# Optimization experiments

Measured on AMD Instinct MI355X. Metric: run time of the kernel, lower is better.

The kernel has to match this reference:

```python
import jax, jax.numpy as jnp
import numpy as np

B, T_ENC, T_DEC = 64, 100, 50
L = 512      # lstm_size
E = 512      # input_encoding_size
H = 512      # att_hidden_size
R = 8        # num_review_steps
V_TOK = 30001  # token_cnt + 1 embedding rows
V_OUT = 30000  # word_cnt


def _lstm_maxout(s, c):
    # ARNet/neuraltalk2 LSTMCore: 5*L preactivations, maxout input transform
    i = jax.nn.sigmoid(s[:, :L])
    f = jax.nn.sigmoid(s[:, L:2 * L])
    o = jax.nn.sigmoid(s[:, 2 * L:3 * L])
    t = jnp.maximum(s[:, 3 * L:4 * L], s[:, 4 * L:])
    c2 = f * c + i * t
    return o * jnp.tanh(c2), c2


def _attend(feats, h, Wa2a, ba2a, Wh2a, bh2a, Watt, batt):
    # feats: [B, A, F], h: [B, L] -> context [B, F]
    p = jnp.tanh(feats @ Wa2a + ba2a + (h @ Wh2a + bh2a)[:, None, :])  # [B,A,H]
    e = jnp.squeeze(p @ Watt, -1) + batt                               # [B,A]
    a = jax.nn.softmax(e, axis=-1)
    return jnp.einsum('ba,baf->bf', a, feats)


def setup_inputs() -> dict:
    key = jax.random.key(0)
    ks = iter(jax.random.split(key, 48))
    g = lambda shape: jax.random.normal(next(ks), shape, jnp.float32) * 0.05
    z = lambda shape: jnp.zeros(shape, jnp.float32)
    return {
        'code_matrix': jax.random.randint(next(ks), (B, T_ENC), 0, V_TOK),
        'comment_matrix': jax.random.randint(next(ks), (B, T_DEC), 0, V_TOK),
        'current_comment_mask_cuda': jnp.ones((B, T_DEC), jnp.float32),
        'embed': jax.random.uniform(next(ks), (V_TOK, E), jnp.float32, -0.1, 0.1),
        'enc_Wi': g((E, 5 * L)), 'enc_bi': z((5 * L,)),
        'enc_Wh': g((L, 5 * L)), 'enc_bh': z((5 * L,)),
        'rev_Wh': g((R, L, 5 * L)), 'rev_bh': z((R, 5 * L)),
        'rev_Wa': g((R, L, 5 * L)), 'rev_ba': z((R, 5 * L)),
        'rev_Wa2a': g((R, L, H)), 'rev_ba2a': z((R, H)),
        'rev_Wh2a': g((R, L, H)), 'rev_bh2a': z((R, H)),
        'rev_Watt': g((R, H, 1)), 'rev_batt': z((R,)),
        'dec_Wi': g((E, 5 * L)), 'dec_bi': z((5 * L,)),
        'dec_Wh': g((L, 5 * L)), 'dec_bh': z((5 * L,)),
        'dec_Wa': g((L, 5 * L)), 'dec_ba': z((5 * L,)),
        'dec_Wa2a': g((L, H)), 'dec_ba2a': z((H,)),
        'dec_Wh2a': g((L, H)), 'dec_bh2a': z((H,)),
        'dec_Watt': g((H, 1)), 'dec_batt': z(()),
        'logit_W': jax.random.uniform(next(ks), (L, V_OUT), jnp.float32, -0.1, 0.1),
        'logit_b': z((V_OUT,)),
    }


def reference(code_matrix, comment_matrix, current_comment_mask_cuda, embed,
              enc_Wi, enc_bi, enc_Wh, enc_bh,
              rev_Wh, rev_bh, rev_Wa, rev_ba, rev_Wa2a, rev_ba2a,
              rev_Wh2a, rev_bh2a, rev_Watt, rev_batt,
              dec_Wi, dec_bi, dec_Wh, dec_bh, dec_Wa, dec_ba,
              dec_Wa2a, dec_ba2a, dec_Wh2a, dec_bh2a, dec_Watt, dec_batt,
              logit_W, logit_b):
    del current_comment_mask_cuda  # only used by scheduled sampling (ss_prob=0)
    Bsz = code_matrix.shape[0]
    h0 = jnp.zeros((Bsz, L), embed.dtype)
    c0 = jnp.zeros((Bsz, L), embed.dtype)

    # ---- encode ----
    enc_x = embed[code_matrix]  # [B, T_enc, E]

    def enc_step(carry, xt):
        h, c = carry
        s = xt @ enc_Wi + enc_bi + h @ enc_Wh + enc_bh
        h2, c2 = _lstm_maxout(s, c)
        return (h2, c2), h2

    (h_enc, c_enc), enc_hs = jax.lax.scan(enc_step, (h0, c0), jnp.swapaxes(enc_x, 0, 1))
    enc_hs = jnp.swapaxes(enc_hs, 0, 1)  # [B, T_enc, L]

    # ---- review (distinct params per step; scan over stacked params) ----
    def rev_step(carry, p):
        h, c = carry
        Wh, bh, Wa, ba, Wa2a, ba2a, Wh2a, bh2a, Watt, batt = p
        att_v = _attend(enc_hs, h, Wa2a, ba2a, Wh2a, bh2a, Watt, batt)
        s = h @ Wh + bh + att_v @ Wa + ba
        h2, c2 = _lstm_maxout(s, c)
        return (h2, c2), h2

    rev_params = (rev_Wh, rev_bh, rev_Wa, rev_ba, rev_Wa2a, rev_ba2a,
                  rev_Wh2a, rev_bh2a, rev_Watt, rev_batt)
    _, thought = jax.lax.scan(rev_step, (h_enc, c_enc), rev_params)
    thought = jnp.swapaxes(thought, 0, 1)  # [B, R, L]

    # ---- decode (teacher forcing; decode_state starts from encode_state) ----
    dec_x = embed[comment_matrix]  # [B, T_dec, E]

    def dec_step(carry, xt):
        h, c = carry
        att_v = _attend(thought, h, dec_Wa2a, dec_ba2a, dec_Wh2a, dec_bh2a, dec_Watt, dec_batt)
        s = xt @ dec_Wi + dec_bi + h @ dec_Wh + dec_bh + att_v @ dec_Wa + dec_ba
        h2, c2 = _lstm_maxout(s, c)
        logp = jax.nn.log_softmax(h2 @ logit_W + logit_b, axis=-1)
        return (h2, c2), logp

    _, logps = jax.lax.scan(dec_step, (h_enc, c_enc), jnp.swapaxes(dec_x, 0, 1))
    return jnp.swapaxes(logps, 0, 1)  # [B, T_dec, V_OUT]
```

## Files before the change

kernel.cpp:

```cpp
#include <hip/hip_runtime.h>
#include <math.h>
#include <stdint.h>

#define BB     64
#define TENC   100
#define TDEC   50
#define LDIM   512
#define EE     512
#define HDIM   512
#define FIVEL  2560
#define RSTEPS 8
#define VOUT   30000
#define NB2    470

typedef __attribute__((ext_vector_type(8))) short short8v;
typedef __attribute__((ext_vector_type(4))) float floatx4;
typedef unsigned short ushort_t;

static const size_t OFF_A        = 0;
static const size_t OFF_WIT_ENC  = 8192000;
static const size_t OFF_ENCX     = 8847360;
static const size_t OFF_LOGWT    = 0;
static const size_t OFF_DECH     = 7680000;
static const size_t OFF_DECPRE   = 8499200;
static const size_t OFF_ENC_HS   = 13107200;
static const size_t OFF_ENC_WHT  = 14745600;
static const size_t OFF_REVWC    = 15400960;
static const size_t OFF_PART     = 15400960;
static const size_t OFF_DECWC    = 25886720;
static const size_t OFF_WIT_DEC  = 27197440;
static const size_t OFF_REVWT    = 27852800;
static const size_t OFF_DECWT    = 28901376;
static const size_t OFF_REVWH2AT = 29032448;
static const size_t OFF_DECWH2AT = 30081024;
static const size_t OFF_DECX     = 30212096;
static const size_t OFF_THOUGHT  = 31031296;
static const size_t OFF_TPROJ    = 31162368;
static const size_t OFF_HB0      = 31293440;
static const size_t OFF_HB1      = 31309824;
static const size_t OFF_ATTV     = 31326208;
static const size_t OFF_H0       = 31342592;
static const size_t OFF_C0       = 31358976;
static const size_t OFF_SBUF     = 31490048;
static const size_t WS_TOTAL     = 31653888;

__device__ __forceinline__ float sigmoidf_(float x) { return 1.0f / (1.0f + __expf(-x)); }
__device__ __forceinline__ float tanh_fast(float x) { return 1.0f - 2.0f / (__expf(2.0f * x) + 1.0f); }
__device__ __forceinline__ unsigned short f2bf(float x) {
    unsigned u = __float_as_uint(x);
    u += 0x7FFFu + ((u >> 16) & 1u);
    return (unsigned short)(u >> 16);
}
__device__ __forceinline__ float bf2f(unsigned short h) {
    return __uint_as_float(((unsigned)h) << 16);
}

__global__ __launch_bounds__(128)
void gather_embed(const float* __restrict__ embed, const int* __restrict__ tok,
                  int T, ushort_t* __restrict__ X)
{
    int m = blockIdx.x, t = m / BB, b = m % BB;
    const float* src = embed + (size_t)tok[b * T + t] * EE;
    float4 v = *(const float4*)(src + threadIdx.x * 4);
    ushort4 o = { f2bf(v.x), f2bf(v.y), f2bf(v.z), f2bf(v.w) };
    *(ushort4*)(X + (size_t)m * EE + threadIdx.x * 4) = o;
}

__global__ __launch_bounds__(256)
void conv_transpose(const float* __restrict__ W, ushort_t* __restrict__ WT,
                    int N, int ldWT, int kofs, long Wz, long WTz)
{
    W  += (size_t)blockIdx.z * Wz;
    WT += (size_t)blockIdx.z * WTz;
    __shared__ float tile[32][33];
    int n0 = blockIdx.x * 32, k0 = blockIdx.y * 32;
    int tx = threadIdx.x & 31, ty = threadIdx.x >> 5;
    #pragma unroll
    for (int i = 0; i < 4; ++i) {
        int k = k0 + ty + i * 8, n = n0 + tx;
        tile[ty + i * 8][tx] = (n < N) ? W[(size_t)k * N + n] : 0.f;
    }
    __syncthreads();
    #pragma unroll
    for (int i = 0; i < 4; ++i) {
        int n = n0 + ty + i * 8, k = k0 + tx;
        if (n < N) WT[(size_t)n * ldWT + kofs + k] = f2bf(tile[tx][ty + i * 8]);
    }
}

__global__ __launch_bounds__(256)
void gemm_bf16(const ushort_t* __restrict__ A, const ushort_t* __restrict__ BT,
               const float* __restrict__ bias, ushort_t* __restrict__ Cb,
               int N, int K, long ldc)
{
    __shared__ ushort_t lds[2][128][32];
    __shared__ ushort_t ctile[128 * 128];
    const int tid  = threadIdx.x;
    const int wave = tid >> 6, lane = tid & 63;
    const int m0 = blockIdx.y * 128, n0 = blockIdx.x * 128;
    const int wr = wave >> 1, wc = wave & 1;

    floatx4 acc[4][4] = {};
    const int sr  = lane >> 2;
    const int scp = lane & 3;

    for (int k0 = 0; k0 < K; k0 += 32) {
        #pragma unroll
        for (int half = 0; half < 2; ++half) {
            int rbase = wave * 32 + half * 16;
            int r = rbase + sr;
            int c = scp ^ ((r >> 1) & 3);
            const ushort_t* ga = A + (size_t)(m0 + r) * K + k0 + c * 8;
            const ushort_t* gb = BT + (size_t)(n0 + r) * K + k0 + c * 8;
            __builtin_amdgcn_global_load_lds(
                (const __attribute__((address_space(1))) void*)ga,
                (__attribute__((address_space(3))) void*)&lds[0][rbase][0], 16, 0, 0);
            __builtin_amdgcn_global_load_lds(
                (const __attribute__((address_space(1))) void*)gb,
                (__attribute__((address_space(3))) void*)&lds[1][rbase][0], 16, 0, 0);
        }
        __syncthreads();

        short8v af[4], bv[4];
        #pragma unroll
        for (int i = 0; i < 4; ++i) {
            int ra = wr * 64 + i * 16 + (lane & 15);
            int ca = (lane >> 4) ^ ((ra >> 1) & 3);
            af[i] = *(const short8v*)&lds[0][ra][ca * 8];
            int rb = wc * 64 + i * 16 + (lane & 15);
            int cb = (lane >> 4) ^ ((rb >> 1) & 3);
            bv[i] = *(const short8v*)&lds[1][rb][cb * 8];
        }
        #pragma unroll
        for (int i = 0; i < 4; ++i)
            #pragma unroll
            for (int j = 0; j < 4; ++j)
                acc[i][j] = __builtin_amdgcn_mfma_f32_16x16x32_bf16(af[i], bv[j], acc[i][j], 0, 0, 0);
        __syncthreads();
    }

    const int crow0 = wr * 64 + (lane >> 4) * 4;
    const int ccol0 = wc * 64 + (lane & 15);
    #pragma unroll
    for (int i = 0; i < 4; ++i) {
        #pragma unroll
        for (int j = 0; j < 4; ++j) {
            int col = ccol0 + j * 16;
            float bval = bias ? bias[n0 + col] : 0.f;
            #pragma unroll
            for (int rr = 0; rr < 4; ++rr)
                ctile[(crow0 + i * 16 + rr) * 128 + col] = f2bf(acc[i][j][rr] + bval);
        }
    }
    __syncthreads();
    #pragma unroll
    for (int itc = 0; itc < 8; ++itc) {
        int chunk = itc * 256 + tid;
        int row = chunk >> 4, ch = chunk & 15;
        *(short8v*)(Cb + (size_t)(m0 + row) * ldc + n0 + ch * 8) =
            *(const short8v*)&ctile[row * 128 + ch * 8];
    }
}

__global__ __launch_bounds__(256)
void gemm_logit(const ushort_t* __restrict__ A, const ushort_t* __restrict__ BT,
                const float* __restrict__ bias, float* __restrict__ C,
                float2* __restrict__ part, int N, int K)
{
    __shared__ ushort_t lds[2][128][32];
    __shared__ float ctf[128 * 128];
    const int tid  = threadIdx.x;
    const int wave = tid >> 6, lane = tid & 63;
    const int m0 = blockIdx.y * 128, n0 = blockIdx.x * 128;
    const int wr = wave >> 1, wc = wave & 1;

    floatx4 acc[4][4] = {};
    const int sr  = lane >> 2;
    const int scp = lane & 3;

    for (int k0 = 0; k0 < K; k0 += 32) {
        #pragma unroll
        for (int half = 0; half < 2; ++half) {
            int rbase = wave * 32 + half * 16;
            int r = rbase + sr;
            int c = scp ^ ((r >> 1) & 3);
            const ushort_t* ga = A + (size_t)(m0 + r) * K + k0 + c * 8;
            int nr = n0 + r; if (nr >= N) nr = 0;
            const ushort_t* gb = BT + (size_t)nr * K + k0 + c * 8;
            __builtin_amdgcn_global_load_lds(
                (const __attribute__((address_space(1))) void*)ga,
                (__attribute__((address_space(3))) void*)&lds[0][rbase][0], 16, 0, 0);
            __builtin_amdgcn_global_load_lds(
                (const __attribute__((address_space(1))) void*)gb,
                (__attribute__((address_space(3))) void*)&lds[1][rbase][0], 16, 0, 0);
        }
        __syncthreads();

        short8v af[4], bv[4];
        #pragma unroll
        for (int i = 0; i < 4; ++i) {
            int ra = wr * 64 + i * 16 + (lane & 15);
            int ca = (lane >> 4) ^ ((ra >> 1) & 3);
            af[i] = *(const short8v*)&lds[0][ra][ca * 8];
            int rb = wc * 64 + i * 16 + (lane & 15);
            int cb = (lane >> 4) ^ ((rb >> 1) & 3);
            bv[i] = *(const short8v*)&lds[1][rb][cb * 8];
        }
        #pragma unroll
        for (int i = 0; i < 4; ++i)
            #pragma unroll
            for (int j = 0; j < 4; ++j)
                acc[i][j] = __builtin_amdgcn_mfma_f32_16x16x32_bf16(af[i], bv[j], acc[i][j], 0, 0, 0);
        __syncthreads();
    }

    const int cn = lane & 15, qq = lane >> 4;
    const int lcol0 = wc * 64 + cn;
    float bv[4]; bool valid[4];
    #pragma unroll
    for (int j = 0; j < 4; ++j) {
        int col = n0 + lcol0 + j * 16;
        valid[j] = col < N;
        bv[j] = valid[j] ? bias[col] : 0.f;
    }
    const int nb2 = blockIdx.x * 2 + wc;
    #pragma unroll
    for (int i = 0; i < 4; ++i) {
        #pragma unroll
        for (int rr = 0; rr < 4; ++rr) {
            int lrow = wr * 64 + qq * 4 + i * 16 + rr;
            int m = m0 + lrow;
            float v[4];
            #pragma unroll
            for (int j = 0; j < 4; ++j)
                v[j] = valid[j] ? acc[i][j][rr] + bv[j] : -3.0e38f;
            float mx = fmaxf(fmaxf(v[0], v[1]), fmaxf(v[2], v[3]));
            #pragma unroll
            for (int msk = 1; msk < 16; msk <<= 1) mx = fmaxf(mx, __shfl_xor(mx, msk));
            float sm = 0.f;
            #pragma unroll
            for (int j = 0; j < 4; ++j) if (valid[j]) sm += __expf(v[j] - mx);
            #pragma unroll
            for (int msk = 1; msk < 16; msk <<= 1) sm += __shfl_xor(sm, msk);
            if (cn == 0) part[(size_t)m * NB2 + nb2] = make_float2(mx, sm);
            #pragma unroll
            for (int j = 0; j < 4; ++j)
                ctf[lrow * 128 + lcol0 + j * 16] = v[j];
        }
    }
    __syncthreads();
    #pragma unroll
    for (int itc = 0; itc < 16; ++itc) {
        int chunk = itc * 256 + tid;
        int row = chunk >> 5, ch = chunk & 31;
        int col = n0 + ch * 4;
        if (col < N) {
            int m = m0 + row;
            int t = m >> 6, bb = m & 63;
            float* dst = C + ((size_t)bb * TDEC + t) * VOUT + col;
            if (col + 3 < N) {
                *(floatx4*)dst = *(const floatx4*)&ctf[row * 128 + ch * 4];
            } else {
                for (int e = 0; e < 4 && col + e < N; ++e)
                    dst[e] = ctf[row * 128 + ch * 4 + e];
            }
        }
    }
}

__global__ __launch_bounds__(256)
void logsm_sub(float* __restrict__ out, const float2* __restrict__ part)
{
    const int r = blockIdx.x;
    const int b = r / TDEC, t = r % TDEC;
    const int m = t * 64 + b;
    const int tid = threadIdx.x, wave = tid >> 6, lane = tid & 63;
    float M = -3.0e38f, S = 0.f;
    for (int i = tid; i < NB2; i += 256) {
        float2 p = part[(size_t)m * NB2 + i];
        float nm = fmaxf(M, p.x);
        S = S * __expf(M - nm) + p.y * __expf(p.x - nm);
        M = nm;
    }
    #pragma unroll
    for (int off = 32; off; off >>= 1) {
        float Mo = __shfl_xor(M, off), So = __shfl_xor(S, off);
        float nm = fmaxf(M, Mo);
        S = S * __expf(M - nm) + So * __expf(Mo - nm);
        M = nm;
    }
    __shared__ float ms[4], ss[4];
    if (lane == 0) { ms[wave] = M; ss[wave] = S; }
    __syncthreads();
    float M2 = fmaxf(fmaxf(ms[0], ms[1]), fmaxf(ms[2], ms[3]));
    float S2 = ss[0] * __expf(ms[0] - M2) + ss[1] * __expf(ms[1] - M2) +
               ss[2] * __expf(ms[2] - M2) + ss[3] * __expf(ms[3] - M2);
    float lse = M2 + __logf(S2);
    floatx4* row = (floatx4*)(out + (size_t)r * VOUT);
    for (int i = tid; i < VOUT / 4; i += 256) {
        floatx4 x = __builtin_nontemporal_load(row + i);
        x[0] -= lse; x[1] -= lse; x[2] -= lse; x[3] -= lse;
        __builtin_nontemporal_store(x, row + i);
    }
}

template<int NSEG>
__global__ __launch_bounds__(256)
void step_gemm(const ushort_t* __restrict__ a0, const ushort_t* __restrict__ a1,
               const ushort_t* __restrict__ BT, int ldBT, float* __restrict__ sbuf)
{
    constexpr int K = NSEG * 512;
    constexpr int LROW = K + 8;
    __shared__ ushort_t Bl[16 * LROW];
    const int tid = threadIdx.x, wave = tid >> 6, lane = tid & 63;
    const int q = lane >> 4, cn = lane & 15;
    const int n0 = blockIdx.x * 16;

    #pragma unroll
    for (int it = 0; it < NSEG * 4; ++it) {
        int slot = it * 4 + wave;
        int row  = slot / NSEG;
        int part = slot % NSEG;
        const ushort_t* src = BT + (size_t)(n0 + row) * ldBT + part * 512 + lane * 8;
        __builtin_amdgcn_global_load_lds(
            (const __attribute__((address_space(1))) void*)src,
            (__attribute__((address_space(3))) void*)&Bl[row * LROW + part * 512], 16, 0, 0);
    }
    __syncthreads();

    floatx4 acc = {0.f, 0.f, 0.f, 0.f};
    {
        const ushort_t* Ap = a0 + (size_t)(wave * 16 + cn) * 512 + q * 8;
        #pragma unroll
        for (int kt = 0; kt < 16; ++kt) {
            short8v af = *(const short8v*)(Ap + kt * 32);
            short8v bf = *(const short8v*)&Bl[cn * LROW + kt * 32 + q * 8];
            acc = __builtin_amdgcn_mfma_f32_16x16x32_bf16(af, bf, acc, 0, 0, 0);
        }
    }
    if (NSEG == 2) {
        const ushort_t* Ap = a1 + (size_t)(wave * 16 + cn) * 512 + q * 8;
        #pragma unroll
        for (int kt = 0; kt < 16; ++kt) {
            short8v af = *(const short8v*)(Ap + kt * 32);
            short8v bf = *(const short8v*)&Bl[cn * LROW + 512 + kt * 32 + q * 8];
            acc = __builtin_amdgcn_mfma_f32_16x16x32_bf16(af, bf, acc, 0, 0, 0);
        }
    }
    #pragma unroll
    for (int rr = 0; rr < 4; ++rr)
        sbuf[(size_t)(wave * 16 + q * 4 + rr) * FIVEL + n0 + cn] = acc[rr];
}

__global__ __launch_bounds__(256)
void lstm_epi(const float* __restrict__ s, const ushort_t* __restrict__ pre,
              const float* __restrict__ b0, const float* __restrict__ b1,
              const float* __restrict__ c_in, float* __restrict__ c_out,
              ushort_t* __restrict__ h_out, ushort_t* __restrict__ h_copy)
{
    int idx = blockIdx.x * 256 + threadIdx.x;
    int row = idx >> 8;
    int c   = (idx & 255) * 2;
    float sg[5][2];
    #pragma unroll
    for (int g = 0; g < 5; ++g) {
        float2 v = *(const float2*)(s + (size_t)row * FIVEL + g * 512 + c);
        sg[g][0] = v.x + b0[g * 512 + c];
        sg[g][1] = v.y + b0[g * 512 + c + 1];
        if (b1) {
            sg[g][0] += b1[g * 512 + c];
            sg[g][1] += b1[g * 512 + c + 1];
        }
        if (pre) {
            ushort2 p = *(const ushort2*)(pre + (size_t)row * FIVEL + g * 512 + c);
            sg[g][0] += bf2f(p.x);
            sg[g][1] += bf2f(p.y);
        }
    }
    float2 ci = *(const float2*)(c_in + (size_t)row * 512 + c);
    float cc[2] = {ci.x, ci.y};
    ushort_t hh[2];
    #pragma unroll
    for (int e = 0; e < 2; ++e) {
        float ig = sigmoidf_(sg[0][e]), fg = sigmoidf_(sg[1][e]), og = sigmoidf_(sg[2][e]);
        float tt = fmaxf(sg[3][e], sg[4][e]);
        float c2 = fg * cc[e] + ig * tt;
        cc[e] = c2;
        hh[e] = f2bf(og * tanh_fast(c2));
    }
    *(float2*)(c_out + (size_t)row * 512 + c) = make_float2(cc[0], cc[1]);
    ushort2 ho = {hh[0], hh[1]};
    *(ushort2*)(h_out + (size_t)row * 512 + c) = ho;
    if (h_copy) *(ushort2*)(h_copy + (size_t)row * 512 + c) = ho;
}

__global__ __launch_bounds__(256)
void attfuse2(const ushort_t* __restrict__ hprev,
              const ushort_t* __restrict__ projBase, long projLd,
              const ushort_t* __restrict__ feats,
              const ushort_t* __restrict__ W2aT, const float* __restrict__ b2a,
              const float* __restrict__ Watt, ushort_t* __restrict__ attv, int A)
{
    __shared__ float hp[512];
    __shared__ float ealpha[128];
    const int b = blockIdx.x;
    const int tid = threadIdx.x, wave = tid >> 6, lane = tid & 63;
    const int q = lane >> 4, cn = lane & 15;

    floatx4 acc[8] = {};
    {
        const ushort_t* Ap = hprev + (size_t)b * 512 + q * 8;
        const ushort_t* Bp = W2aT + (size_t)(wave * 128 + cn) * 512 + q * 8;
        #pragma unroll 2
        for (int kt = 0; kt < 16; ++kt) {
            short8v af = *(const short8v*)(Ap + kt * 32);
            #pragma unroll
            for (int t8 = 0; t8 < 8; ++t8) {
                short8v bf = *(const short8v*)(Bp + (size_t)t8 * 16 * 512 + kt * 32);
                acc[t8] = __builtin_amdgcn_mfma_f32_16x16x32_bf16(af, bf, acc[t8], 0, 0, 0);
            }
        }
    }
    if (q == 0) {
        #pragma unroll
        for (int t8 = 0; t8 < 8; ++t8) {
            int n = wave * 128 + t8 * 16 + cn;
            hp[n] = acc[t8][0] + b2a[n];
        }
    }
    __syncthreads();

    float hpr[8], war[8];
    {
        float4 w0 = *(const float4*)(Watt + lane * 8);
        float4 w1 = *(const float4*)(Watt + lane * 8 + 4);
        war[0] = w0.x; war[1] = w0.y; war[2] = w0.z; war[3] = w0.w;
        war[4] = w1.x; war[5] = w1.y; war[6] = w1.z; war[7] = w1.w;
        #pragma unroll
        for (int j = 0; j < 8; ++j) hpr[j] = hp[lane * 8 + j];
    }

    for (int a = wave; a < A; a += 4) {
        short8v pv = *(const short8v*)(projBase + ((size_t)a * 64 + b) * projLd + lane * 8);
        float e = 0.f;
        #pragma unroll
        for (int j = 0; j < 8; ++j)
            e += tanh_fast(bf2f((ushort_t)pv[j]) + hpr[j]) * war[j];
        #pragma unroll
        for (int off = 32; off; off >>= 1) e += __shfl_xor(e, off);
        if (lane == 0) ealpha[a] = e;
    }
    __syncthreads();
    if (wave == 0) {
        float v1 = (lane < A) ? ealpha[lane] : -3.0e38f;
        float v2 = (lane + 64 < A) ? ealpha[lane + 64] : -3.0e38f;
        float mm = fmaxf(v1, v2);
        #pragma unroll
        for (int off = 32; off; off >>= 1) mm = fmaxf(mm, __shfl_xor(mm, off));
        float x1 = (lane < A) ? __expf(v1 - mm) : 0.f;
        float x2 = (lane + 64 < A) ? __expf(v2 - mm) : 0.f;
        float ss = x1 + x2;
        #pragma unroll
        for (int off = 32; off; off >>= 1) ss += __shfl_xor(ss, off);
        float inv = 1.f / ss;
        if (lane < A) ealpha[lane] = x1 * inv;
        if (lane + 64 < A) ealpha[lane + 64] = x2 * inv;
    }
    __syncthreads();

    float s0 = 0.f, s1 = 0.f;
    for (int a = 0; a < A; ++a) {
        float al = ealpha[a];
        unsigned int u = *(const unsigned int*)(feats + ((size_t)a * 64 + b) * 512 + tid * 2);
        s0 += al * bf2f((ushort_t)(u & 0xffffu));
        s1 += al * bf2f((ushort_t)(u >> 16));
    }
    ushort2 o = { f2bf(s0), f2bf(s1) };
    *(ushort2*)(attv + (size_t)b * 512 + tid * 2) = o;
}

extern "C" void kernel_launch(void* const* d_in, const int* in_sizes, int n_in,
                              void* d_out_, int out_size, void* d_ws, size_t ws_size,
                              hipStream_t stream)
{
    const int*   code     = (const int*)  d_in[0];
    const int*   comment  = (const int*)  d_in[1];
    const float* embed    = (const float*)d_in[3];
    const float* enc_Wi   = (const float*)d_in[4];
    const float* enc_bi   = (const float*)d_in[5];
    const float* enc_Wh   = (const float*)d_in[6];
    const float* enc_bh   = (const float*)d_in[7];
    const float* rev_Wh   = (const float*)d_in[8];
    const float* rev_bh   = (const float*)d_in[9];
    const float* rev_Wa   = (const float*)d_in[10];
    const float* rev_ba   = (const float*)d_in[11];
    const float* rev_Wa2a = (const float*)d_in[12];
    const float* rev_ba2a = (const float*)d_in[13];
    const float* rev_Wh2a = (const float*)d_in[14];
    const float* rev_bh2a = (const float*)d_in[15];
    const float* rev_Watt = (const float*)d_in[16];
    const float* dec_Wi   = (const float*)d_in[18];
    const float* dec_bi   = (const float*)d_in[19];
    const float* dec_Wh   = (const float*)d_in[20];
    const float* dec_bh   = (const float*)d_in[21];
    const float* dec_Wa   = (const float*)d_in[22];
    const float* dec_ba   = (const float*)d_in[23];
    const float* dec_Wa2a = (const float*)d_in[24];
    const float* dec_ba2a = (const float*)d_in[25];
    const float* dec_Wh2a = (const float*)d_in[26];
    const float* dec_bh2a = (const float*)d_in[27];
    const float* dec_Watt = (const float*)d_in[28];
    const float* logit_W  = (const float*)d_in[30];
    const float* logit_b  = (const float*)d_in[31];
    float* out = (float*)d_out_;

    float* ws = (float*)d_ws;
    if (ws_size < WS_TOTAL * sizeof(float)) return;

    ushort_t* enc_pre_b = (ushort_t*)(ws + OFF_A);
    ushort_t* rev_projA = (ushort_t*)(ws + OFF_A);
    ushort_t* logit_WT  = (ushort_t*)(ws + OFF_LOGWT);
    ushort_t* dec_h_b   = (ushort_t*)(ws + OFF_DECH);
    ushort_t* dec_pre_b = (ushort_t*)(ws + OFF_DECPRE);
    ushort_t* WiT_enc   = (ushort_t*)(ws + OFF_WIT_ENC);
    ushort_t* enc_x_b   = (ushort_t*)(ws + OFF_ENCX);
    ushort_t* enc_hs_b  = (ushort_t*)(ws + OFF_ENC_HS);
    ushort_t* encWhT    = (ushort_t*)(ws + OFF_ENC_WHT);
    ushort_t* revWcomb  = (ushort_t*)(ws + OFF_REVWC);
    float2*   part      = (float2*)(ws + OFF_PART);
    ushort_t* decWcomb  = (ushort_t*)(ws + OFF_DECWC);
    ushort_t* WiT_dec   = (ushort_t*)(ws + OFF_WIT_DEC);
    ushort_t* revWT     = (ushort_t*)(ws + OFF_REVWT);
    ushort_t* decWT     = (ushort_t*)(ws + OFF_DECWT);
    ushort_t* revWh2aT  = (ushort_t*)(ws + OFF_REVWH2AT);
    ushort_t* decWh2aT  = (ushort_t*)(ws + OFF_DECWH2AT);
    ushort_t* dec_x_b   = (ushort_t*)(ws + OFF_DECX);
    ushort_t* thought_b = (ushort_t*)(ws + OFF_THOUGHT);
    ushort_t* tproj_b   = (ushort_t*)(ws + OFF_TPROJ);
    ushort_t* hb[2] = { (ushort_t*)(ws + OFF_HB0), (ushort_t*)(ws + OFF_HB1) };
    ushort_t* attv_b    = (ushort_t*)(ws + OFF_ATTV);
    ushort_t* h0_b      = (ushort_t*)(ws + OFF_H0);
    float*    sbuf      = ws + OFF_SBUF;
    float* cbuf[4];
    for (int i = 0; i < 4; ++i) cbuf[i] = ws + OFF_C0 + (size_t)i * 32768;

    const dim3 blk(256);

    (void)hipMemsetAsync(cbuf[0], 0, (size_t)BB * LDIM * sizeof(float), stream);
    (void)hipMemsetAsync(h0_b, 0, (size_t)BB * LDIM * sizeof(ushort_t), stream);

    gather_embed<<<TENC * BB, 128, 0, stream>>>(embed, code, TENC, enc_x_b);
    gather_embed<<<TDEC * BB, 128, 0, stream>>>(embed, comment, TDEC, dec_x_b);
    conv_transpose<<<dim3(80, 16, 1), blk, 0, stream>>>(enc_Wi, WiT_enc, FIVEL, 512, 0, 0, 0);
    conv_transpose<<<dim3(80, 16, 1), blk, 0, stream>>>(enc_Wh, encWhT, FIVEL, 512, 0, 0, 0);
    conv_transpose<<<dim3(80, 16, 8), blk, 0, stream>>>(rev_Wh, revWcomb, FIVEL, 1024, 0,   1310720, 2621440);
    conv_transpose<<<dim3(80, 16, 8), blk, 0, stream>>>(rev_Wa, revWcomb, FIVEL, 1024, 512, 1310720, 2621440);
    conv_transpose<<<dim3(16, 16, 8), blk, 0, stream>>>(rev_Wa2a, revWT, 512, 512, 0,       262144, 262144);
    conv_transpose<<<dim3(16, 16, 8), blk, 0, stream>>>(rev_Wh2a, revWh2aT, 512, 512, 0,    262144, 262144);
    conv_transpose<<<dim3(80, 16, 1), blk, 0, stream>>>(dec_Wi, WiT_dec, FIVEL, 512, 0, 0, 0);
    conv_transpose<<<dim3(80, 16, 1), blk, 0, stream>>>(dec_Wh, decWcomb, FIVEL, 1024, 0, 0, 0);
    conv_transpose<<<dim3(80, 16, 1), blk, 0, stream>>>(dec_Wa, decWcomb, FIVEL, 1024, 512, 0, 0);
    conv_transpose<<<dim3(16, 16, 1), blk, 0, stream>>>(dec_Wa2a, decWT, 512, 512, 0, 0, 0);
    conv_transpose<<<dim3(16, 16, 1), blk, 0, stream>>>(dec_Wh2a, decWh2aT, 512, 512, 0, 0, 0);

    gemm_bf16<<<dim3(FIVEL / 128, TENC * BB / 128), blk, 0, stream>>>(
        enc_x_b, WiT_enc, enc_bi, enc_pre_b, FIVEL, EE, FIVEL);

    for (int t = 0; t < TENC; ++t) {
        const ushort_t* hin = (t == 0) ? h0_b : enc_hs_b + (size_t)(t - 1) * 32768;
        step_gemm<1><<<160, blk, 0, stream>>>(hin, nullptr, encWhT, 512, sbuf);
        lstm_epi<<<64, blk, 0, stream>>>(
            sbuf, enc_pre_b + (size_t)t * 163840, enc_bh, nullptr,
            cbuf[t & 1], cbuf[(t + 1) & 1],
            enc_hs_b + (size_t)t * 32768, nullptr);
    }
    const ushort_t* h_enc = enc_hs_b + (size_t)(TENC - 1) * 32768;

    gemm_bf16<<<dim3(32, 50), blk, 0, stream>>>(
        enc_hs_b, revWT, rev_ba2a, rev_projA, 4096, LDIM, 4096);

    const ushort_t* rh = h_enc;
    for (int r = 0; r < RSTEPS; ++r) {
        attfuse2<<<BB, blk, 0, stream>>>(
            rh, rev_projA + (size_t)r * 512, 4096, enc_hs_b,
            revWh2aT + (size_t)r * 262144, rev_bh2a + (size_t)r * 512,
            rev_Watt + (size_t)r * 512, attv_b, TENC);
        step_gemm<2><<<160, blk, 0, stream>>>(
            rh, attv_b, revWcomb + (size_t)r * 2621440, 1024, sbuf);
        const float* ci = (r == 0) ? cbuf[0] : cbuf[2 + ((r - 1) & 1)];
        lstm_epi<<<64, blk, 0, stream>>>(
            sbuf, nullptr, rev_bh + (size_t)r * FIVEL, rev_ba + (size_t)r * FIVEL,
            ci, cbuf[2 + (r & 1)],
            hb[r & 1], thought_b + (size_t)r * 32768);
        rh = hb[r & 1];
    }

    gemm_bf16<<<dim3(4, 4), blk, 0, stream>>>(
        thought_b, decWT, dec_ba2a, tproj_b, HDIM, LDIM, HDIM);
    conv_transpose<<<dim3((VOUT + 31) / 32, 16, 1), blk, 0, stream>>>(
        logit_W, logit_WT, VOUT, 512, 0, 0, 0);
    gemm_bf16<<<dim3(FIVEL / 128, TDEC * BB / 128), blk, 0, stream>>>(
        dec_x_b, WiT_dec, dec_bi, dec_pre_b, FIVEL, EE, FIVEL);

    const ushort_t* dh = h_enc;
    for (int t = 0; t < TDEC; ++t) {
        attfuse2<<<BB, blk, 0, stream>>>(
            dh, tproj_b, 512, thought_b,
            decWh2aT, dec_bh2a, dec_Watt, attv_b, RSTEPS);
        step_gemm<2><<<160, blk, 0, stream>>>(
            dh, attv_b, decWcomb, 1024, sbuf);
        const float* ci = (t == 0) ? cbuf[0] : cbuf[2 + ((t - 1) & 1)];
        lstm_epi<<<64, blk, 0, stream>>>(
            sbuf, dec_pre_b + (size_t)t * 163840, dec_bh, dec_ba,
            ci, cbuf[2 + (t & 1)],
            hb[t & 1], dec_h_b + (size_t)t * 32768);
        dh = hb[t & 1];
    }

    gemm_logit<<<dim3(235, 25), blk, 0, stream>>>(
        dec_h_b, logit_WT, logit_b, out, part, VOUT, LDIM);
    logsm_sub<<<TDEC * BB, blk, 0, stream>>>(out, part);
}
```

Baseline: 3.450 ms.

## Fuse attention into LSTM epilogue and precompute thought×Wa projection for decoder

Folds the attention computation for the next step into the LSTM epilogue kernel, removing one launch per review and decode step. In the decoder, the context-vector GEMM is replaced by precomputing thought·dec_Wa once (TPW), so each step only mixes eight projected rows by the attention weights, and the step GEMM shrinks to K=512. The logit GEMM is also remapped to a 1D grid with an XCD-aware tile order for better L2 locality. The epilogue now does more serial work per block on only 64 blocks, and TPW reuses the encoder-states workspace region, which depends on that buffer being dead by then.

```diff
diff --git a/kernel.cpp b/kernel.cpp
--- a/kernel.cpp
+++ b/kernel.cpp
@@ -24,6 +24,7 @@
 static const size_t OFF_DECH     = 7680000;
 static const size_t OFF_DECPRE   = 8499200;
 static const size_t OFF_ENC_HS   = 13107200;
+static const size_t OFF_TPW      = 13107200;
 static const size_t OFF_ENC_WHT  = 14745600;
 static const size_t OFF_REVWC    = 15400960;
 static const size_t OFF_PART     = 15400960;
@@ -42,7 +43,8 @@
 static const size_t OFF_H0       = 31342592;
 static const size_t OFF_C0       = 31358976;
 static const size_t OFF_SBUF     = 31490048;
-static const size_t WS_TOTAL     = 31653888;
+static const size_t OFF_ALPHA    = 31653888;
+static const size_t WS_TOTAL     = 31654400;
 
 __device__ __forceinline__ float sigmoidf_(float x) { return 1.0f / (1.0f + __expf(-x)); }
 __device__ __forceinline__ float tanh_fast(float x) { return 1.0f - 2.0f / (__expf(2.0f * x) + 1.0f); }
@@ -171,7 +173,11 @@
     __shared__ float ctf[128 * 128];
     const int tid  = threadIdx.x;
     const int wave = tid >> 6, lane = tid & 63;
-    const int m0 = blockIdx.y * 128, n0 = blockIdx.x * 128;
+    int lin = blockIdx.x;
+    int xcd = lin & 7, o = lin >> 3;
+    int wgid = (xcd < 3 ? xcd * 735 + o : 3 * 735 + (xcd - 3) * 734 + o);
+    const int ntile = wgid / 25, mtile = wgid % 25;
+    const int m0 = mtile * 128, n0 = ntile * 128;
     const int wr = wave >> 1, wc = wave & 1;
 
     floatx4 acc[4][4] = {};
@@ -223,7 +229,7 @@
         valid[j] = col < N;
         bv[j] = valid[j] ? bias[col] : 0.f;
     }
-    const int nb2 = blockIdx.x * 2 + wc;
+    const int nb2 = ntile * 2 + wc;
     #pragma unroll
     for (int i = 0; i < 4; ++i) {
         #pragma unroll
@@ -392,6 +398,154 @@
     ushort2 ho = {hh[0], hh[1]};
     *(ushort2*)(h_out + (size_t)row * 512 + c) = ho;
     if (h_copy) *(ushort2*)(h_copy + (size_t)row * 512 + c) = ho;
+}
+
+__global__ __launch_bounds__(256)
+void epi_att(const float* __restrict__ s, const ushort_t* __restrict__ hprev,
+             const ushort_t* __restrict__ pre,
+             const float* __restrict__ b0, const float* __restrict__ b1,
+             const ushort_t* __restrict__ tpw, const float* __restrict__ alpha_in,
+             const float* __restrict__ c_in, float* __restrict__ c_out,
+             ushort_t* __restrict__ h_out, ushort_t* __restrict__ h_copy,
+             const ushort_t* __restrict__ projBase, long projLd,
+             const ushort_t* __restrict__ feats,
+             const ushort_t* __restrict__ W2aT, const float* __restrict__ b2a,
+             const float* __restrict__ Watt,
+             ushort_t* __restrict__ attv_out, float* __restrict__ alphas_out, int A)
+{
+    __shared__ ushort_t hl[512];
+    __shared__ float hp[512];
+    __shared__ float ealpha[128];
+    const int b = blockIdx.x;
+    const int tid = threadIdx.x, wave = tid >> 6, lane = tid & 63;
+
+    if (s) {
+        const int c = tid * 2;
+        float al[8];
+        if (tpw) {
+            #pragma unroll
+            for (int a = 0; a < 8; ++a) al[a] = alpha_in[b * 8 + a];
+        }
+        float sg[5][2];
+        #pragma unroll
+        for (int g = 0; g < 5; ++g) {
+            float2 v = *(const float2*)(s + (size_t)b * FIVEL + g * 512 + c);
+            sg[g][0] = v.x + b0[g * 512 + c];
+            sg[g][1] = v.y + b0[g * 512 + c + 1];
+            if (b1) {
+                sg[g][0] += b1[g * 512 + c];
+                sg[g][1] += b1[g * 512 + c + 1];
+            }
+            if (pre) {
+                ushort2 p = *(const ushort2*)(pre + (size_t)b * FIVEL + g * 512 + c);
+                sg[g][0] += bf2f(p.x);
+                sg[g][1] += bf2f(p.y);
+            }
+            if (tpw) {
+                #pragma unroll
+                for (int a = 0; a < 8; ++a) {
+                    ushort2 tv = *(const ushort2*)(tpw + ((size_t)a * 64 + b) * FIVEL + g * 512 + c);
+                    sg[g][0] += al[a] * bf2f(tv.x);
+                    sg[g][1] += al[a] * bf2f(tv.y);
+                }
+            }
+        }
+        float2 ci = *(const float2*)(c_in + (size_t)b * 512 + c);
+        float cc[2] = {ci.x, ci.y};
+        ushort_t hh[2];
+        #pragma unroll
+        for (int e = 0; e < 2; ++e) {
+            float ig = sigmoidf_(sg[0][e]), fg = sigmoidf_(sg[1][e]), og = sigmoidf_(sg[2][e]);
+            float tt = fmaxf(sg[3][e], sg[4][e]);
+            float c2 = fg * cc[e] + ig * tt;
+            cc[e] = c2;
+            hh[e] = f2bf(og * tanh_fast(c2));
+        }
+        *(float2*)(c_out + (size_t)b * 512 + c) = make_float2(cc[0], cc[1]);
+        ushort2 ho = {hh[0], hh[1]};
+        *(ushort2*)(h_out + (size_t)b * 512 + c) = ho;
+        if (h_copy) *(ushort2*)(h_copy + (size_t)b * 512 + c) = ho;
+        *(ushort2*)&hl[c] = ho;
+    } else {
+        *(ushort2*)&hl[tid * 2] = *(const ushort2*)(hprev + (size_t)b * 512 + tid * 2);
+    }
+    if (!W2aT) return;
+    __syncthreads();
+
+    const int q = lane >> 4, cn = lane & 15;
+    floatx4 acc[8] = {};
+    {
+        const ushort_t* Bp = W2aT + (size_t)(wave * 128 + cn) * 512 + q * 8;
+        #pragma unroll 2
+        for (int kt = 0; kt < 16; ++kt) {
+            short8v af = *(const short8v*)&hl[kt * 32 + q * 8];
+            #pragma unroll
+            for (int t8 = 0; t8 < 8; ++t8) {
+                short8v bf = *(const short8v*)(Bp + (size_t)t8 * 16 * 512 + kt * 32);
+                acc[t8] = __builtin_amdgcn_mfma_f32_16x16x32_bf16(af, bf, acc[t8], 0, 0, 0);
+            }
+        }
+    }
+    if (q == 0) {
+        #pragma unroll
+        for (int t8 = 0; t8 < 8; ++t8) {
+            int n = wave * 128 + t8 * 16 + cn;
+            hp[n] = acc[t8][0] + b2a[n];
+        }
+    }
+    __syncthreads();
+
+    float hpr[8], war[8];
+    {
+        float4 w0 = *(const float4*)(Watt + lane * 8);
+        float4 w1 = *(const float4*)(Watt + lane * 8 + 4);
+        war[0] = w0.x; war[1] = w0.y; war[2] = w0.z; war[3] = w0.w;
+        war[4] = w1.x; war[5] = w1.y; war[6] = w1.z; war[7] = w1.w;
+        #pragma unroll
+        for (int j = 0; j < 8; ++j) hpr[j] = hp[lane * 8 + j];
+    }
+
+    for (int a = wave; a < A; a += 4) {
+        short8v pv = *(const short8v*)(projBase + ((size_t)a * 64 + b) * projLd + lane * 8);
+        float e = 0.f;
+        #pragma unroll
+        for (int j = 0; j < 8; ++j)
+            e += tanh_fast(bf2f((ushort_t)pv[j]) + hpr[j]) * war[j];
+        #pragma unroll
+        for (int off = 32; off; off >>= 1) e += __shfl_xor(e, off);
+        if (lane == 0) ealpha[a] = e;
+    }
+    __syncthreads();
+    if (wave == 0) {
+        float v1 = (lane < A) ? ealpha[lane] : -3.0e38f;
+        float v2 = (lane + 64 < A) ? ealpha[lane + 64] : -3.0e38f;
+        float mm = fmaxf(v1, v2);
+        #pragma unroll
+        for (int off = 32; off; off >>= 1) mm = fmaxf(mm, __shfl_xor(mm, off));
+        float x1 = (lane < A) ? __expf(v1 - mm) : 0.f;
+        float x2 = (lane + 64 < A) ? __expf(v2 - mm) : 0.f;
+        float ss = x1 + x2;
+        #pragma unroll
+        for (int off = 32; off; off >>= 1) ss += __shfl_xor(ss, off);
+        float inv = 1.f / ss;
+        if (lane < A) ealpha[lane] = x1 * inv;
+        if (lane + 64 < A) ealpha[lane + 64] = x2 * inv;
+    }
+    __syncthreads();
+
+    if (attv_out) {
+        float s0 = 0.f, s1 = 0.f;
+        for (int a = 0; a < A; ++a) {
+            float alv = ealpha[a];
+            unsigned int u = *(const unsigned int*)(feats + ((size_t)a * 64 + b) * 512 + tid * 2);
+            s0 += alv * bf2f((ushort_t)(u & 0xffffu));
+            s1 += alv * bf2f((ushort_t)(u >> 16));
+        }
+        ushort2 o = { f2bf(s0), f2bf(s1) };
+        *(ushort2*)(attv_out + (size_t)b * 512 + tid * 2) = o;
+    } else {
+        if (tid < A) alphas_out[b * A + tid] = ealpha[tid];
+    }
 }
 
 __global__ __launch_bounds__(256)
@@ -525,10 +679,12 @@
     ushort_t* WiT_enc   = (ushort_t*)(ws + OFF_WIT_ENC);
     ushort_t* enc_x_b   = (ushort_t*)(ws + OFF_ENCX);
     ushort_t* enc_hs_b  = (ushort_t*)(ws + OFF_ENC_HS);
+    ushort_t* TPW       = (ushort_t*)(ws + OFF_TPW);
     ushort_t* encWhT    = (ushort_t*)(ws + OFF_ENC_WHT);
     ushort_t* revWcomb  = (ushort_t*)(ws + OFF_REVWC);
     float2*   part      = (float2*)(ws + OFF_PART);
-    ushort_t* decWcomb  = (ushort_t*)(ws + OFF_DECWC);
+    ushort_t* decWhT    = (ushort_t*)(ws + OFF_DECWC);
+    ushort_t* WaT_dec   = (ushort_t*)(ws + OFF_DECWC + 655360);
     ushort_t* WiT_dec   = (ushort_t*)(ws + OFF_WIT_DEC);
     ushort_t* revWT     = (ushort_t*)(ws + OFF_REVWT);
     ushort_t* decWT     = (ushort_t*)(ws + OFF_DECWT);
@@ -541,6 +697,7 @@
     ushort_t* attv_b    = (ushort_t*)(ws + OFF_ATTV);
     ushort_t* h0_b      = (ushort_t*)(ws + OFF_H0);
     float*    sbuf      = ws + OFF_SBUF;
+    float*    alphas    = ws + OFF_ALPHA;
     float* cbuf[4];
     for (int i = 0; i < 4; ++i) cbuf[i] = ws + OFF_C0 + (size_t)i * 32768;
 
@@ -558,8 +715,8 @@
     conv_transpose<<<dim3(16, 16, 8), blk, 0, stream>>>(rev_Wa2a, revWT, 512, 512, 0,       262144, 262144);
     conv_transpose<<<dim3(16, 16, 8), blk, 0, stream>>>(rev_Wh2a, revWh2aT, 512, 512, 0,    262144, 262144);
     conv_transpose<<<dim3(80, 16, 1), blk, 0, stream>>>(dec_Wi, WiT_dec, FIVEL, 512, 0, 0, 0);
-    conv_transpose<<<dim3(80, 16, 1), blk, 0, stream>>>(dec_Wh, decWcomb, FIVEL, 1024, 0, 0, 0);
-    conv_transpose<<<dim3(80, 16, 1), blk, 0, stream>>>(dec_Wa, decWcomb, FIVEL, 1024, 512, 0, 0);
+    conv_transpose<<<dim3(80, 16, 1), blk, 0, stream>>>(dec_Wh, decWhT, FIVEL, 512, 0, 0, 0);
+    conv_transpose<<<dim3(80, 16, 1), blk, 0, stream>>>(dec_Wa, WaT_dec, FIVEL, 512, 0, 0, 0);
     conv_transpose<<<dim3(16, 16, 1), blk, 0, stream>>>(dec_Wa2a, decWT, 512, 512, 0, 0, 0);
     conv_transpose<<<dim3(16, 16, 1), blk, 0, stream>>>(dec_Wh2a, decWh2aT, 512, 512, 0, 0, 0);
 
@@ -579,19 +736,24 @@
     gemm_bf16<<<dim3(32, 50), blk, 0, stream>>>(
         enc_hs_b, revWT, rev_ba2a, rev_projA, 4096, LDIM, 4096);
 
+    attfuse2<<<BB, blk, 0, stream>>>(
+        h_enc, rev_projA, 4096, enc_hs_b,
+        revWh2aT, rev_bh2a, rev_Watt, attv_b, TENC);
     const ushort_t* rh = h_enc;
     for (int r = 0; r < RSTEPS; ++r) {
-        attfuse2<<<BB, blk, 0, stream>>>(
-            rh, rev_projA + (size_t)r * 512, 4096, enc_hs_b,
-            revWh2aT + (size_t)r * 262144, rev_bh2a + (size_t)r * 512,
-            rev_Watt + (size_t)r * 512, attv_b, TENC);
         step_gemm<2><<<160, blk, 0, stream>>>(
             rh, attv_b, revWcomb + (size_t)r * 2621440, 1024, sbuf);
         const float* ci = (r == 0) ? cbuf[0] : cbuf[2 + ((r - 1) & 1)];
-        lstm_epi<<<64, blk, 0, stream>>>(
-            sbuf, nullptr, rev_bh + (size_t)r * FIVEL, rev_ba + (size_t)r * FIVEL,
+        const ushort_t* nextW = (r < RSTEPS - 1) ? revWh2aT + (size_t)(r + 1) * 262144 : nullptr;
+        epi_att<<<BB, blk, 0, stream>>>(
+            sbuf, nullptr, nullptr,
+            rev_bh + (size_t)r * FIVEL, rev_ba + (size_t)r * FIVEL,
+            nullptr, nullptr,
             ci, cbuf[2 + (r & 1)],
-            hb[r & 1], thought_b + (size_t)r * 32768);
+            hb[r & 1], thought_b + (size_t)r * 32768,
+            rev_projA + (size_t)(r + 1) * 512, 4096, enc_hs_b,
+            nextW, rev_bh2a + (size_t)(r + 1) * 512, rev_Watt + (size_t)(r + 1) * 512,
+            attv_b, nullptr, TENC);
         rh = hb[r & 1];
     }
 
@@ -601,23 +763,30 @@
         logit_W, logit_WT, VOUT, 512, 0, 0, 0);
     gemm_bf16<<<dim3(FIVEL / 128, TDEC * BB / 128), blk, 0, stream>>>(
         dec_x_b, WiT_dec, dec_bi, dec_pre_b, FIVEL, EE, FIVEL);
-
-    const ushort_t* dh = h_enc;
+    gemm_bf16<<<dim3(20, 4), blk, 0, stream>>>(
+        thought_b, WaT_dec, nullptr, TPW, FIVEL, LDIM, FIVEL);
+
+    epi_att<<<BB, blk, 0, stream>>>(
+        nullptr, h_enc, nullptr, nullptr, nullptr, nullptr, nullptr,
+        nullptr, nullptr, nullptr, nullptr,
+        tproj_b, 512, nullptr,
+        decWh2aT, dec_bh2a, dec_Watt, nullptr, alphas, RSTEPS);
     for (int t = 0; t < TDEC; ++t) {
-        attfuse2<<<BB, blk, 0, stream>>>(
-            dh, tproj_b, 512, thought_b,
-            decWh2aT, dec_bh2a, dec_Watt, attv_b, RSTEPS);
-        step_gemm<2><<<160, blk, 0, stream>>>(
-            dh, attv_b, decWcomb, 1024, sbuf);
+        const ushort_t* dh = (t == 0) ? h_enc : hb[(t - 1) & 1];
+        step_gemm<1><<<160, blk, 0, stream>>>(dh, nullptr, decWhT, 512, sbuf);
         const float* ci = (t == 0) ? cbuf[0] : cbuf[2 + ((t - 1) & 1)];
-        lstm_epi<<<64, blk, 0, stream>>>(
-            sbuf, dec_pre_b + (size_t)t * 163840, dec_bh, dec_ba,
+        const ushort_t* nextW = (t < TDEC - 1) ? decWh2aT : nullptr;
+        epi_att<<<BB, blk, 0, stream>>>(
+            sbuf, nullptr, dec_pre_b + (size_t)t * 163840,
+            dec_bh, dec_ba,
+            TPW, alphas,
             ci, cbuf[2 + (t & 1)],
-            hb[t & 1], dec_h_b + (size_t)t * 32768);
-        dh = hb[t & 1];
-    }
-
-    gemm_logit<<<dim3(235, 25), blk, 0, stream>>>(
+            hb[t & 1], dec_h_b + (size_t)t * 32768,
+            tproj_b, 512, nullptr,
+            nextW, dec_bh2a, dec_Watt, nullptr, alphas, RSTEPS);
+    }
+
+    gemm_logit<<<dim3(235 * 25), blk, 0, stream>>>(
         dec_h_b, logit_WT, logit_b, out, part, VOUT, LDIM);
     logsm_sub<<<TDEC * BB, blk, 0, stream>>>(out, part);
 }
```

New measurement: 3.351 ms. -2.9%, faster.
